# Kernel tuning notes

Hardware: AMD Instinct MI355X
Metric: run time of the kernel (lower is better)

## Reference

```python
import jax, jax.numpy as jnp
import numpy as np
import math

DIM = 1024
MLP = 4096
D_STATE = 16
D_CONV = 4
EXPAND = 2
D_INNER = EXPAND * DIM
HALF = D_INNER // 2
DT_RANK = math.ceil(DIM / 16)
BSZ = 2
SEQ = 2048
LN_EPS = 1e-5


def setup_inputs() -> dict:
    key = jax.random.key(0)
    ks = jax.random.split(key, 12)
    s = lambda k, shape, sc: jax.random.normal(k, shape, dtype=jnp.float32) * sc
    return {
        "x": s(ks[0], (BSZ, SEQ, DIM), 1.0),
        "ln1_g": jnp.ones((DIM,), jnp.float32),
        "ln1_b": jnp.zeros((DIM,), jnp.float32),
        "in_proj_w": s(ks[1], (D_INNER, DIM), 0.02),
        "conv_x_w": s(ks[2], (HALF, 1, D_CONV), 0.1),
        "conv_x_b": jnp.zeros((HALF,), jnp.float32),
        "conv_z_w": s(ks[3], (HALF, 1, D_CONV), 0.1),
        "conv_z_b": jnp.zeros((HALF,), jnp.float32),
        "x_proj_w": s(ks[4], (DT_RANK + 2 * D_STATE, HALF), 0.02),
        "dt_proj_w": s(ks[5], (HALF, DT_RANK), 0.02),
        "dt_proj_b": s(ks[6], (HALF,), 0.1),
        "A_log": jnp.log(jnp.tile(jnp.arange(1, D_STATE + 1, dtype=jnp.float32), (HALF, 1))),
        "Dp": jnp.ones((HALF,), jnp.float32),
        "out_proj_w": s(ks[7], (DIM, D_INNER), 0.02),
        "ln2_g": jnp.ones((DIM,), jnp.float32),
        "ln2_b": jnp.zeros((DIM,), jnp.float32),
        "mlp_w1": s(ks[8], (MLP, DIM), 0.02),
        "mlp_b1": jnp.zeros((MLP,), jnp.float32),
        "mlp_w2": s(ks[9], (DIM, MLP), 0.02),
        "mlp_b2": jnp.zeros((DIM,), jnp.float32),
    }


def _ln(x, g, b):
    mu = jnp.mean(x, -1, keepdims=True)
    v = jnp.mean((x - mu) ** 2, -1, keepdims=True)
    return (x - mu) * jax.lax.rsqrt(v + LN_EPS) * g + b


def _dwconv_same(x, w, b):
    # x: [B, C, L]; w: [C, 1, K] depthwise; PyTorch 'same' pads left=(K-1)//2, right=rest
    total = D_CONV - 1
    left = total // 2
    y = jax.lax.conv_general_dilated(
        x, w, (1,), [(left, total - left)],
        dimension_numbers=("NCH", "OIH", "NCH"),
        feature_group_count=x.shape[1])
    return y + b[None, :, None]


def _mixer(x, in_proj_w, conv_x_w, conv_x_b, conv_z_w, conv_z_b,
           x_proj_w, dt_proj_w, dt_proj_b, A_log, Dp, out_proj_w):
    Bsz = x.shape[0]
    xz = jnp.einsum('bld,ed->ble', x, in_proj_w)              # [B,L,2*HALF]
    xs, zs = jnp.split(xz, 2, axis=-1)
    xc = jax.nn.silu(_dwconv_same(jnp.swapaxes(xs, 1, 2), conv_x_w, conv_x_b))  # [B,HALF,L]
    zc = jax.nn.silu(_dwconv_same(jnp.swapaxes(zs, 1, 2), conv_z_w, conv_z_b))  # [B,HALF,L]
    u = jnp.swapaxes(xc, 1, 2)                                 # [B,L,HALF]
    x_dbl = jnp.einsum('bld,ed->ble', u, x_proj_w)             # [B,L,dt_rank+2N]
    dt, Bm, Cm = jnp.split(x_dbl, [DT_RANK, DT_RANK + D_STATE], axis=-1)
    delta = jax.nn.softplus(jnp.einsum('blr,dr->bld', dt, dt_proj_w) + dt_proj_b)  # [B,L,HALF]
    A = -jnp.exp(A_log)                                        # [HALF,N]
    dA = jnp.exp(jnp.einsum('bld,dn->lbdn', delta, A))         # [L,B,HALF,N]
    dBu = jnp.einsum('bld,bln,bld->lbdn', delta, Bm, u)        # [L,B,HALF,N]
    Cs = jnp.moveaxis(Cm, 1, 0)                                # [L,B,N]

    def step(h, t):
        dA_t, dBu_t, c_t = t
        h = dA_t * h + dBu_t                                   # [B,HALF,N]
        return h, jnp.einsum('bdn,bn->bd', h, c_t)

    h0 = jnp.zeros((Bsz, HALF, D_STATE), x.dtype)
    _, ys = jax.lax.scan(step, h0, (dA, dBu, Cs))              # ys: [L,B,HALF]
    y = jnp.moveaxis(ys, 0, 1) + u * Dp                        # [B,L,HALF]
    y = jnp.concatenate([y, jnp.swapaxes(zc, 1, 2)], axis=-1)  # [B,L,2*HALF]
    return jnp.einsum('ble,de->bld', y, out_proj_w)


def reference(x, ln1_g, ln1_b, in_proj_w, conv_x_w, conv_x_b, conv_z_w, conv_z_b,
              x_proj_w, dt_proj_w, dt_proj_b, A_log, Dp, out_proj_w,
              ln2_g, ln2_b, mlp_w1, mlp_b1, mlp_w2, mlp_b2):
    x = x + _mixer(_ln(x, ln1_g, ln1_b), in_proj_w, conv_x_w, conv_x_b,
                   conv_z_w, conv_z_b, x_proj_w, dt_proj_w, dt_proj_b,
                   A_log, Dp, out_proj_w)
    h = _ln(x, ln2_g, ln2_b)
    h = jax.nn.gelu(jnp.einsum('bld,md->blm', h, mlp_w1) + mlp_b1, approximate=False)
    h = jnp.einsum('blm,dm->bld', h, mlp_w2) + mlp_b2
    return x + h
```

## Files before the change

### kernel.cpp

```cpp
#include <hip/hip_runtime.h>
#include <math.h>

#define DIMD    1024
#define MLPD    4096
#define DSTATE  16
#define DCONV   4
#define HALF    1024
#define DINNER  2048
#define DTRANK  64
#define BSZ     2
#define SEQ     2048
#define NTOK    (BSZ*SEQ)
#define NCH     64
#define CL      (SEQ/NCH)

typedef short bf16x8 __attribute__((ext_vector_type(8)));
typedef float f32x4  __attribute__((ext_vector_type(4)));
typedef float f32x16 __attribute__((ext_vector_type(16)));
typedef unsigned short u16;
typedef unsigned int   u32;
typedef unsigned short u16x4 __attribute__((ext_vector_type(4)));

__device__ __forceinline__ u16 f2bf(float x) {
    union { float f; unsigned int u; } v; v.f = x;
    unsigned int r = (v.u + 0x7FFFu + ((v.u >> 16) & 1u)) >> 16;
    return (u16)r;
}
__device__ __forceinline__ float bf2f(u16 x) {
    union { unsigned int u; float f; } v; v.u = ((unsigned int)x) << 16;
    return v.f;
}

#define SZ_WIN  (DINNER*DIMD)
#define SZ_WXP  (96*HALF)
#define SZ_WDT  (HALF*DTRANK)
#define SZ_WOUT (DIMD*DINNER)
#define SZ_WM1  (MLPD*DIMD)
#define SZ_WM2  (DIMD*MLPD)
#define SZ_TOT  (SZ_WIN+SZ_WXP+SZ_WDT+SZ_WOUT+SZ_WM1+SZ_WM2)
#define CVT_BLOCKS (SZ_TOT / 1024)

__global__ __launch_bounds__(256) void cvtln_kernel(
        const float* __restrict__ x, const float* __restrict__ g,
        const float* __restrict__ b, u16* __restrict__ xn_bf,
        const float* __restrict__ s0, u16* __restrict__ d0,
        const float* __restrict__ s1, u16* __restrict__ d1,
        const float* __restrict__ s2, u16* __restrict__ d2,
        const float* __restrict__ s3, u16* __restrict__ d3,
        const float* __restrict__ s4, u16* __restrict__ d4,
        const float* __restrict__ s5, u16* __restrict__ d5) {
    if (blockIdx.x >= NTOK) {
        int i = (blockIdx.x - NTOK) * 1024 + threadIdx.x * 4;
        #define CVT4(s, d) { \
            float4 v = *(const float4*)((s) + i); \
            u16x4 o; o[0]=f2bf(v.x); o[1]=f2bf(v.y); o[2]=f2bf(v.z); o[3]=f2bf(v.w); \
            *(u16x4*)((d) + i) = o; }
        if (i < SZ_WIN)  { CVT4(s0, d0); return; }  i -= SZ_WIN;
        if (i < SZ_WXP)  { CVT4(s1, d1); return; }  i -= SZ_WXP;
        if (i < SZ_WDT)  { CVT4(s2, d2); return; }  i -= SZ_WDT;
        if (i < SZ_WOUT) { CVT4(s3, d3); return; }  i -= SZ_WOUT;
        if (i < SZ_WM1)  { CVT4(s4, d4); return; }  i -= SZ_WM1;
        if (i < SZ_WM2)  { CVT4(s5, d5); }
        #undef CVT4
        return;
    }
    __shared__ float sm[4];
    int row = blockIdx.x;
    int t = threadIdx.x;
    const float4* xr = (const float4*)(x + (size_t)row * DIMD);
    float4 v = xr[t];
    float s = v.x + v.y + v.z + v.w;
    for (int off = 32; off > 0; off >>= 1) s += __shfl_down(s, off, 64);
    if ((t & 63) == 0) sm[t >> 6] = s;
    __syncthreads();
    float mu = (sm[0] + sm[1] + sm[2] + sm[3]) * (1.0f / DIMD);
    float dx = v.x - mu, dy = v.y - mu, dz = v.z - mu, dw = v.w - mu;
    float ss = dx*dx + dy*dy + dz*dz + dw*dw;
    for (int off = 32; off > 0; off >>= 1) ss += __shfl_down(ss, off, 64);
    __syncthreads();
    if ((t & 63) == 0) sm[t >> 6] = ss;
    __syncthreads();
    float var = (sm[0] + sm[1] + sm[2] + sm[3]) * (1.0f / DIMD);
    float rs = rsqrtf(var + 1e-5f);
    float4 gv = ((const float4*)g)[t];
    float4 bv = ((const float4*)b)[t];
    u16* o = xn_bf + (size_t)row * DIMD + t * 4;
    o[0] = f2bf(dx * rs * gv.x + bv.x);
    o[1] = f2bf(dy * rs * gv.y + bv.y);
    o[2] = f2bf(dz * rs * gv.z + bv.z);
    o[3] = f2bf(dw * rs * gv.w + bv.w);
}

__global__ __launch_bounds__(256) void gemm_small_kernel(
        const u16* __restrict__ A, int lda,
        const u16* __restrict__ W, int K, int N,
        float* __restrict__ Cf, u16* __restrict__ Cb) {
    __shared__ f32x4 red[2][64];
    int t = threadIdx.x;
    int w = t >> 6, lane = t & 63;
    int mt = w & 1, kh = w >> 1;
    int m0 = blockIdx.x * 32 + mt * 16;
    int n0 = blockIdx.y * 16;
    int r = lane & 15, quad = lane >> 4;
    int Kh = K >> 1;
    f32x4 acc = {0.f, 0.f, 0.f, 0.f};
    const u16* ap = A + (size_t)(m0 + r) * lda + kh * Kh + quad * 8;
    const u16* wp = W + (size_t)(n0 + r) * K   + kh * Kh + quad * 8;
    for (int k = 0; k < Kh; k += 32) {
        bf16x8 av = *(const bf16x8*)(ap + k);
        bf16x8 bv = *(const bf16x8*)(wp + k);
        acc = __builtin_amdgcn_mfma_f32_16x16x32_bf16(av, bv, acc, 0, 0, 0);
    }
    if (kh == 1) red[mt][lane] = acc;
    __syncthreads();
    if (kh == 0) {
        f32x4 o = red[mt][lane];
        int col = n0 + r;
        #pragma unroll
        for (int i = 0; i < 4; ++i) {
            int row = m0 + quad * 4 + i;
            size_t idx = (size_t)row * N + col;
            float v = acc[i] + o[i];
            Cf[idx] = v;
            Cb[idx] = f2bf(v);
        }
    }
}

template<int EPI, int TN, int KS>
__global__ __launch_bounds__(256) void gemm128_kernel(
        const u16* __restrict__ A, int lda, const u16* __restrict__ W,
        int K, int N,
        const float* __restrict__ bias, const float* __restrict__ resid,
        float* __restrict__ Cf, float* __restrict__ Cf2,
        u16* __restrict__ Cb) {
    constexpr int NF = TN / 32;
    constexpr int NN = TN / 64;
    __shared__ u16 As0[128 * 32], As1[128 * 32];
    __shared__ u16 Bs0[TN * 32],  Bs1[TN * 32];
    const int t = threadIdx.x;
    const int w = t >> 6;
    const int lane = t & 63;
    const int r32 = lane & 31;
    const int kh  = lane >> 5;
    const int wm = w & 1, wn = w >> 1;
    const int m0 = blockIdx.x * 128;
    const int n0 = blockIdx.y * TN;
    const int Kloc = K / KS;
    const int kz = (KS == 2) ? blockIdx.z : 0;

    f32x16 acc[2][NN];
    #pragma unroll
    for (int mi = 0; mi < 2; ++mi)
        #pragma unroll
        for (int ni = 0; ni < NN; ++ni)
            acc[mi][ni] = (f32x16){0.f,0.f,0.f,0.f,0.f,0.f,0.f,0.f,
                                   0.f,0.f,0.f,0.f,0.f,0.f,0.f,0.f};

    const u16* pa[2];
    const u16* pb[NF / 2];
    #pragma unroll
    for (int i = 0; i < 2; ++i) {
        int c = (i * 4 + w) * 64 + lane;
        int row = c >> 2;
        int q = (c & 3) ^ ((row >> 1) & 3);
        pa[i] = A + (size_t)(m0 + row) * lda + (size_t)kz * Kloc + q * 8;
    }
    #pragma unroll
    for (int i = 0; i < NF / 2; ++i) {
        int c = (i * 4 + w) * 64 + lane;
        int row = c >> 2;
        int q = (c & 3) ^ ((row >> 1) & 3);
        pb[i] = W + (size_t)(n0 + row) * K + (size_t)kz * Kloc + q * 8;
    }
    const int gsw = (r32 >> 1) & 3;
    int aoff[2][2], boff[NN][2];
    #pragma unroll
    for (int mi = 0; mi < 2; ++mi)
        #pragma unroll
        for (int tt = 0; tt < 2; ++tt)
            aoff[mi][tt] = (wm * 64 + mi * 32 + r32) * 32 +
                           ((tt * 2 + kh) ^ gsw) * 8;
    #pragma unroll
    for (int ni = 0; ni < NN; ++ni)
        #pragma unroll
        for (int tt = 0; tt < 2; ++tt)
            boff[ni][tt] = (wn * (TN / 2) + ni * 32 + r32) * 32 +
                           ((tt * 2 + kh) ^ gsw) * 8;

    auto stage = [&](u16* __restrict__ Ad, u16* __restrict__ Bd) {
        #pragma unroll
        for (int i = 0; i < 2; ++i) {
            __builtin_amdgcn_global_load_lds(
                (const __attribute__((address_space(1))) u32*)pa[i],
                (__attribute__((address_space(3))) u32*)(Ad + (i * 4 + w) * 512),
                16, 0, 0);
            pa[i] += 32;
        }
        #pragma unroll
        for (int i = 0; i < NF / 2; ++i) {
            __builtin_amdgcn_global_load_lds(
                (const __attribute__((address_space(1))) u32*)pb[i],
                (__attribute__((address_space(3))) u32*)(Bd + (i * 4 + w) * 512),
                16, 0, 0);
            pb[i] += 32;
        }
    };
    auto compute = [&](const u16* __restrict__ Ab, const u16* __restrict__ Bb) {
        bf16x8 af[2][2], bfr[NN][2];
        #pragma unroll
        for (int mi = 0; mi < 2; ++mi)
            #pragma unroll
            for (int tt = 0; tt < 2; ++tt)
                af[mi][tt] = *(const bf16x8*)(Ab + aoff[mi][tt]);
        #pragma unroll
        for (int ni = 0; ni < NN; ++ni)
            #pragma unroll
            for (int tt = 0; tt < 2; ++tt)
                bfr[ni][tt] = *(const bf16x8*)(Bb + boff[ni][tt]);
        #pragma unroll
        for (int tt = 0; tt < 2; ++tt)
            #pragma unroll
            for (int mi = 0; mi < 2; ++mi)
                #pragma unroll
                for (int ni = 0; ni < NN; ++ni)
                    acc[mi][ni] = __builtin_amdgcn_mfma_f32_32x32x16_bf16(
                        af[mi][tt], bfr[ni][tt], acc[mi][ni], 0, 0, 0);
    };

    stage(As0, Bs0);
    for (int k0 = 0; k0 < Kloc; k0 += 64) {
        __syncthreads();
        if (k0 + 32 < Kloc) stage(As1, Bs1);
        compute(As0, Bs0);
        __syncthreads();
        if (k0 + 64 < Kloc) stage(As0, Bs0);
        compute(As1, Bs1);
    }

    float* Cfo = (KS == 2 && kz) ? Cf2 : Cf;
    #pragma unroll
    for (int mi = 0; mi < 2; ++mi) {
        #pragma unroll
        for (int ni = 0; ni < NN; ++ni) {
            #pragma unroll
            for (int reg = 0; reg < 16; ++reg) {
                int row = m0 + wm * 64 + mi * 32 + (reg & 3) + 8 * (reg >> 2) + 4 * kh;
                int col = n0 + wn * (TN / 2) + ni * 32 + r32;
                size_t idx = (size_t)row * N + col;
                float v = acc[mi][ni][reg];
                if (EPI == 1) { v += bias[col]; v = (v > 20.f) ? v : log1pf(expf(v)); }
                if (EPI == 2) {
                    v += bias[col];
                    float e = __expf(fminf(1.5957691216f * v + 0.0713548162f * v * v * v, 80.f));
                    v = v * __fdividef(e, e + 1.f);
                }
                if (EPI == 3) { v += resid[idx]; }
                if (EPI == 4) { v += bias[col] + resid[idx]; }
                if (EPI == 2 || EPI == 5) Cb[idx] = f2bf(v);
                else                      Cfo[idx] = v;
            }
        }
    }
}

__global__ __launch_bounds__(256) void reduce2_kernel(
        const float* __restrict__ P0, const float* __restrict__ P1,
        const float* __restrict__ bias, const float* __restrict__ resid,
        float* __restrict__ out) {
    size_t idx = ((size_t)blockIdx.x * 256 + threadIdx.x) * 4;
    float4 a = *(const float4*)(P0 + idx);
    float4 b = *(const float4*)(P1 + idx);
    float4 rr = *(const float4*)(resid + idx);
    int col = (int)(idx & (DIMD - 1));
    float4 bb = *(const float4*)(bias + col);
    float4 o;
    o.x = a.x + b.x + rr.x + bb.x;
    o.y = a.y + b.y + rr.y + bb.y;
    o.z = a.z + b.z + rr.z + bb.z;
    o.w = a.w + b.w + rr.w + bb.w;
    *(float4*)(out + idx) = o;
}

__global__ __launch_bounds__(256) void reduce_ln_kernel(
        const float* __restrict__ P0, const float* __restrict__ P1,
        const float* __restrict__ resid,
        const float* __restrict__ g, const float* __restrict__ b,
        float* __restrict__ x2, u16* __restrict__ out_bf) {
    __shared__ float sm[4];
    int row = blockIdx.x;
    int t = threadIdx.x;
    size_t base = (size_t)row * DIMD + t * 4;
    float4 a  = *(const float4*)(P0 + base);
    float4 p  = *(const float4*)(P1 + base);
    float4 rr = *(const float4*)(resid + base);
    float4 v;
    v.x = a.x + p.x + rr.x;
    v.y = a.y + p.y + rr.y;
    v.z = a.z + p.z + rr.z;
    v.w = a.w + p.w + rr.w;
    *(float4*)(x2 + base) = v;
    float s = v.x + v.y + v.z + v.w;
    for (int off = 32; off > 0; off >>= 1) s += __shfl_down(s, off, 64);
    if ((t & 63) == 0) sm[t >> 6] = s;
    __syncthreads();
    float mu = (sm[0] + sm[1] + sm[2] + sm[3]) * (1.0f / DIMD);
    float dx = v.x - mu, dy = v.y - mu, dz = v.z - mu, dw = v.w - mu;
    float ss = dx*dx + dy*dy + dz*dz + dw*dw;
    for (int off = 32; off > 0; off >>= 1) ss += __shfl_down(ss, off, 64);
    __syncthreads();
    if ((t & 63) == 0) sm[t >> 6] = ss;
    __syncthreads();
    float var = (sm[0] + sm[1] + sm[2] + sm[3]) * (1.0f / DIMD);
    float rs = rsqrtf(var + 1e-5f);
    float4 gv = ((const float4*)g)[t];
    float4 bv = ((const float4*)b)[t];
    u16* o = out_bf + base;
    o[0] = f2bf(dx * rs * gv.x + bv.x);
    o[1] = f2bf(dy * rs * gv.y + bv.y);
    o[2] = f2bf(dz * rs * gv.z + bv.z);
    o[3] = f2bf(dw * rs * gv.w + bv.w);
}

__global__ __launch_bounds__(256) void conv_silu_kernel(
        const u16* __restrict__ xz,
        const float* __restrict__ wx, const float* __restrict__ bx,
        const float* __restrict__ wz, const float* __restrict__ bz,
        u16* __restrict__ u_bf, u16* __restrict__ ycat) {
    int c  = blockIdx.x * 256 + threadIdx.x;
    int gy = blockIdx.y;
    int b  = gy >> 8;
    int l0 = (gy & 255) * 8;
    const u16* base = xz + ((size_t)(b * SEQ + l0)) * DINNER;
    float wxr[4], wzr[4];
    #pragma unroll
    for (int k = 0; k < 4; ++k) { wxr[k] = wx[c * 4 + k]; wzr[k] = wz[c * 4 + k]; }
    float bxv = bx[c], bzv = bz[c];
    float xm1 = (l0 > 0) ? bf2f(base[c - DINNER]) : 0.f;
    float x0v = bf2f(base[c]);
    float x1v = bf2f(base[c + DINNER]);
    float zm1 = (l0 > 0) ? bf2f(base[HALF + c - DINNER]) : 0.f;
    float z0v = bf2f(base[HALF + c]);
    float z1v = bf2f(base[HALF + c + DINNER]);
    u16* up = u_bf + ((size_t)(b * SEQ + l0)) * HALF + c;
    u16* yp = ycat + ((size_t)(b * SEQ + l0)) * DINNER + HALF + c;
    #pragma unroll
    for (int l = 0; l < 8; ++l) {
        bool in = (l0 + l + 2) < SEQ;
        float x2v = in ? bf2f(base[(size_t)(l + 2) * DINNER + c]) : 0.f;
        float z2v = in ? bf2f(base[(size_t)(l + 2) * DINNER + HALF + c]) : 0.f;
        float ax = bxv + wxr[0]*xm1 + wxr[1]*x0v + wxr[2]*x1v + wxr[3]*x2v;
        float az = bzv + wzr[0]*zm1 + wzr[1]*z0v + wzr[2]*z1v + wzr[3]*z2v;
        float sx = ax * __fdividef(1.f, 1.f + __expf(-ax));
        float sz = az * __fdividef(1.f, 1.f + __expf(-az));
        *up = f2bf(sx); *yp = f2bf(sz);
        up += HALF; yp += DINNER;
        xm1 = x0v; x0v = x1v; x1v = x2v;
        zm1 = z0v; z0v = z1v; z1v = z2v;
    }
}

__global__ __launch_bounds__(256) void scan_p1_kernel(
        const float* __restrict__ delta, const u16* __restrict__ u_bf,
        const float* __restrict__ x_dbl, const float* __restrict__ A_log,
        float* __restrict__ hfin, float* __restrict__ dsum) {
    int t  = blockIdx.x * 256 + threadIdx.x;
    int d  = t & (HALF - 1);
    int ch = (t >> 10) & (NCH - 1);
    int b  = t >> 16;
    float Ac[16], h[16];
    #pragma unroll
    for (int i = 0; i < 4; ++i) {
        float4 a = *(const float4*)&A_log[d * DSTATE + i * 4];
        Ac[4*i+0] = -__expf(a.x); Ac[4*i+1] = -__expf(a.y);
        Ac[4*i+2] = -__expf(a.z); Ac[4*i+3] = -__expf(a.w);
        h[4*i+0] = 0.f; h[4*i+1] = 0.f; h[4*i+2] = 0.f; h[4*i+3] = 0.f;
    }
    int l0 = b * SEQ + ch * CL;
    size_t off = (size_t)l0 * HALF + d;
    const float* xrow = x_dbl + (size_t)l0 * 96;
    float ds = 0.f;
    #pragma unroll 4
    for (int l = 0; l < CL; ++l) {
        float dl = delta[off];
        float uv = bf2f(u_bf[off]);
        off += HALF;
        float4 B0 = *(const float4*)(xrow + 64);
        float4 B1 = *(const float4*)(xrow + 68);
        float4 B2 = *(const float4*)(xrow + 72);
        float4 B3 = *(const float4*)(xrow + 76);
        xrow += 96;
        float dBu = dl * uv;
        ds += dl;
        float Bv[16] = {B0.x,B0.y,B0.z,B0.w, B1.x,B1.y,B1.z,B1.w,
                        B2.x,B2.y,B2.z,B2.w, B3.x,B3.y,B3.z,B3.w};
        #pragma unroll
        for (int n = 0; n < 16; ++n)
            h[n] = __expf(dl * Ac[n]) * h[n] + dBu * Bv[n];
    }
    float4* hf = (float4*)&hfin[(size_t)t * 16];
    #pragma unroll
    for (int i = 0; i < 4; ++i)
        hf[i] = (float4){h[4*i+0], h[4*i+1], h[4*i+2], h[4*i+3]};
    dsum[t] = ds;
}

__global__ __launch_bounds__(256) void scan_p2_kernel(
        const float* __restrict__ A_log, const float* __restrict__ dsum,
        const float* __restrict__ hfin, float* __restrict__ hin) {
    int t = blockIdx.x * 256 + threadIdx.x;
    int n = t & 15;
    int d = (t >> 4) & (HALF - 1);
    int b = t >> 14;
    float Ac = -__expf(A_log[d * DSTATE + n]);
    float h = 0.f;
    for (int ch = 0; ch < NCH; ++ch) {
        size_t chain = ((size_t)(b * NCH + ch) * HALF) + d;
        hin[chain * 16 + n] = h;
        float ds = dsum[chain];
        h = __expf(Ac * ds) * h + hfin[chain * 16 + n];
    }
}

__global__ __launch_bounds__(256) void scan_p3_kernel(
        const float* __restrict__ delta, const u16* __restrict__ u_bf,
        const float* __restrict__ x_dbl, const float* __restrict__ A_log,
        const float* __restrict__ Dp, const float* __restrict__ hin,
        u16* __restrict__ ycat) {
    int t  = blockIdx.x * 256 + threadIdx.x;
    int d  = t & (HALF - 1);
    int ch = (t >> 10) & (NCH - 1);
    int b  = t >> 16;
    float Ac[16], h[16];
    #pragma unroll
    for (int i = 0; i < 4; ++i) {
        float4 a  = *(const float4*)&A_log[d * DSTATE + i * 4];
        float4 hv = *(const float4*)&hin[(size_t)t * 16 + i * 4];
        Ac[4*i+0] = -__expf(a.x); Ac[4*i+1] = -__expf(a.y);
        Ac[4*i+2] = -__expf(a.z); Ac[4*i+3] = -__expf(a.w);
        h[4*i+0] = hv.x; h[4*i+1] = hv.y; h[4*i+2] = hv.z; h[4*i+3] = hv.w;
    }
    float Dv = Dp[d];
    int l0 = b * SEQ + ch * CL;
    size_t off = (size_t)l0 * HALF + d;
    const float* xrow = x_dbl + (size_t)l0 * 96;
    u16* yp = ycat + (size_t)l0 * DINNER + d;
    #pragma unroll 4
    for (int l = 0; l < CL; ++l) {
        float dl = delta[off];
        float uv = bf2f(u_bf[off]);
        off += HALF;
        float4 B0 = *(const float4*)(xrow + 64);
        float4 B1 = *(const float4*)(xrow + 68);
        float4 B2 = *(const float4*)(xrow + 72);
        float4 B3 = *(const float4*)(xrow + 76);
        float4 C0 = *(const float4*)(xrow + 80);
        float4 C1 = *(const float4*)(xrow + 84);
        float4 C2 = *(const float4*)(xrow + 88);
        float4 C3 = *(const float4*)(xrow + 92);
        xrow += 96;
        float dBu = dl * uv;
        float Bv[16] = {B0.x,B0.y,B0.z,B0.w, B1.x,B1.y,B1.z,B1.w,
                        B2.x,B2.y,B2.z,B2.w, B3.x,B3.y,B3.z,B3.w};
        float Cv[16] = {C0.x,C0.y,C0.z,C0.w, C1.x,C1.y,C1.z,C1.w,
                        C2.x,C2.y,C2.z,C2.w, C3.x,C3.y,C3.z,C3.w};
        float y = uv * Dv;
        #pragma unroll
        for (int n = 0; n < 16; ++n) {
            h[n] = __expf(dl * Ac[n]) * h[n] + dBu * Bv[n];
            y += h[n] * Cv[n];
        }
        *yp = f2bf(y);
        yp += DINNER;
    }
}

extern "C" void kernel_launch(void* const* d_in, const int* in_sizes, int n_in,
                              void* d_out, int out_size, void* d_ws, size_t ws_size,
                              hipStream_t stream) {
    const float* x         = (const float*)d_in[0];
    const float* ln1_g     = (const float*)d_in[1];
    const float* ln1_b     = (const float*)d_in[2];
    const float* in_proj_w = (const float*)d_in[3];
    const float* conv_x_w  = (const float*)d_in[4];
    const float* conv_x_b  = (const float*)d_in[5];
    const float* conv_z_w  = (const float*)d_in[6];
    const float* conv_z_b  = (const float*)d_in[7];
    const float* x_proj_w  = (const float*)d_in[8];
    const float* dt_proj_w = (const float*)d_in[9];
    const float* dt_proj_b = (const float*)d_in[10];
    const float* A_log     = (const float*)d_in[11];
    const float* Dp        = (const float*)d_in[12];
    const float* out_proj_w= (const float*)d_in[13];
    const float* ln2_g     = (const float*)d_in[14];
    const float* ln2_b     = (const float*)d_in[15];
    const float* mlp_w1    = (const float*)d_in[16];
    const float* mlp_b1    = (const float*)d_in[17];
    const float* mlp_w2    = (const float*)d_in[18];
    const float* mlp_b2    = (const float*)d_in[19];
    float* out = (float*)d_out;

    char* p = (char*)d_ws;
    auto alloc = [&](size_t bytes) {
        char* r = p; p += (bytes + 255) & ~(size_t)255; return r;
    };
    u16*   w_in   = (u16*)  alloc((size_t)DINNER * DIMD * 2);
    u16*   w_xp   = (u16*)  alloc((size_t)96 * HALF * 2);
    u16*   w_dt   = (u16*)  alloc((size_t)HALF * DTRANK * 2);
    u16*   w_out  = (u16*)  alloc((size_t)DIMD * DINNER * 2);
    u16*   w_m1   = (u16*)  alloc((size_t)MLPD * DIMD * 2);
    u16*   w_m2   = (u16*)  alloc((size_t)DIMD * MLPD * 2);
    u16*   xn_bf  = (u16*)  alloc((size_t)NTOK * DIMD * 2);
    u16*   xz_bf  = (u16*)  alloc((size_t)NTOK * DINNER * 2);
    u16*   u_bf   = (u16*)  alloc((size_t)NTOK * HALF * 2);
    u16*   ycat   = (u16*)  alloc((size_t)NTOK * DINNER * 2);
    float* x_dbl  = (float*)alloc((size_t)NTOK * 96 * 4);
    u16*   xdbl_bf= (u16*)  alloc((size_t)NTOK * 96 * 2);
    float* delta  = (float*)alloc((size_t)NTOK * HALF * 4);
    float* x2     = (float*)alloc((size_t)NTOK * DIMD * 4);
    u16*   ln2_bf = (u16*)  alloc((size_t)NTOK * DIMD * 2);
    u16*   mlp_h  = (u16*)  alloc((size_t)NTOK * MLPD * 2);
    float* hfin = (float*)mlp_h;
    float* hin  = hfin + (size_t)BSZ * NCH * HALF * DSTATE;
    float* dsum = hin  + (size_t)BSZ * NCH * HALF * DSTATE;
    float* P0 = delta;
    float* P1 = (float*)xz_bf;

    cvtln_kernel<<<NTOK + CVT_BLOCKS, 256, 0, stream>>>(
        x, ln1_g, ln1_b, xn_bf,
        in_proj_w, w_in, x_proj_w, w_xp, dt_proj_w, w_dt,
        out_proj_w, w_out, mlp_w1, w_m1, mlp_w2, w_m2);

    gemm128_kernel<5,128,1><<<dim3(NTOK/128, DINNER/128), 256, 0, stream>>>(
        xn_bf, DIMD, w_in, DIMD, DINNER, nullptr, nullptr, nullptr, nullptr, xz_bf);

    conv_silu_kernel<<<dim3(HALF/256, NTOK/8), 256, 0, stream>>>(
        xz_bf, conv_x_w, conv_x_b, conv_z_w, conv_z_b, u_bf, ycat);

    gemm_small_kernel<<<dim3(NTOK/32, 96/16), 256, 0, stream>>>(
        u_bf, HALF, w_xp, HALF, 96, x_dbl, xdbl_bf);

    gemm128_kernel<1,64,1><<<dim3(NTOK/128, HALF/64), 256, 0, stream>>>(
        xdbl_bf, 96, w_dt, DTRANK, HALF, dt_proj_b, nullptr, delta, nullptr, nullptr);

    scan_p1_kernel<<<(BSZ*NCH*HALF)/256, 256, 0, stream>>>(
        delta, u_bf, x_dbl, A_log, hfin, dsum);
    scan_p2_kernel<<<(BSZ*HALF*DSTATE)/256, 256, 0, stream>>>(
        A_log, dsum, hfin, hin);
    scan_p3_kernel<<<(BSZ*NCH*HALF)/256, 256, 0, stream>>>(
        delta, u_bf, x_dbl, A_log, Dp, hin, ycat);

    gemm128_kernel<0,128,2><<<dim3(NTOK/128, DIMD/128, 2), 256, 0, stream>>>(
        ycat, DINNER, w_out, DINNER, DIMD, nullptr, nullptr, P0, P1, nullptr);
    reduce_ln_kernel<<<NTOK, 256, 0, stream>>>(
        P0, P1, x, ln2_g, ln2_b, x2, ln2_bf);

    gemm128_kernel<2,128,1><<<dim3(NTOK/128, MLPD/128), 256, 0, stream>>>(
        ln2_bf, DIMD, w_m1, DIMD, MLPD, mlp_b1, nullptr, nullptr, nullptr, mlp_h);

    gemm128_kernel<0,128,2><<<dim3(NTOK/128, DIMD/128, 2), 256, 0, stream>>>(
        mlp_h, MLPD, w_m2, MLPD, DIMD, nullptr, nullptr, P0, P1, nullptr);
    reduce2_kernel<<<(NTOK*DIMD)/1024, 256, 0, stream>>>(
        P0, P1, mlp_b2, x2, out);
}
```

Before: 413.0 us.

## Triple-buffer GEMM shared-memory tiles with partial vmcnt waits

Moves the bf16 GEMM main loop from double to triple buffering of the A/B LDS tiles, staging two tiles ahead. Plain __syncthreads are replaced by explicit s_waitcnt vmcnt(N) followed by a raw barrier, so that global loads for the next stage can stay in flight while the current tile is computed. The cost is more LDS per block, which may reduce occupancy. Correctness also depends on the hand-counted vmcnt values matching the number of loads issued per stage.

```diff
diff --git a/kernel.cpp b/kernel.cpp
--- a/kernel.cpp
+++ b/kernel.cpp
@@ -136,8 +136,8 @@
         u16* __restrict__ Cb) {
     constexpr int NF = TN / 32;
     constexpr int NN = TN / 64;
-    __shared__ u16 As0[128 * 32], As1[128 * 32];
-    __shared__ u16 Bs0[TN * 32],  Bs1[TN * 32];
+    __shared__ u16 As0[128 * 32], As1[128 * 32], As2[128 * 32];
+    __shared__ u16 Bs0[TN * 32],  Bs1[TN * 32],  Bs2[TN * 32];
     const int t = threadIdx.x;
     const int w = t >> 6;
     const int lane = t & 63;
@@ -227,15 +227,35 @@
                     acc[mi][ni] = __builtin_amdgcn_mfma_f32_32x32x16_bf16(
                         af[mi][tt], bfr[ni][tt], acc[mi][ni], 0, 0, 0);
     };
+    auto waitbar = [&](bool last) {
+        if (last) {
+            asm volatile("s_waitcnt vmcnt(0)" ::: "memory");
+        } else if constexpr (TN == 128) {
+            asm volatile("s_waitcnt vmcnt(4)" ::: "memory");
+        } else {
+            asm volatile("s_waitcnt vmcnt(3)" ::: "memory");
+        }
+        __builtin_amdgcn_s_barrier();
+        __builtin_amdgcn_sched_barrier(0);
+    };
 
     stage(As0, Bs0);
-    for (int k0 = 0; k0 < Kloc; k0 += 64) {
-        __syncthreads();
-        if (k0 + 32 < Kloc) stage(As1, Bs1);
+    stage(As1, Bs1);
+    const int NT = Kloc / 32;
+    int it = 0;
+    while (true) {
+        waitbar(it == NT - 1);
+        if (it + 2 < NT) stage(As2, Bs2);
         compute(As0, Bs0);
-        __syncthreads();
-        if (k0 + 64 < Kloc) stage(As0, Bs0);
+        if (++it >= NT) break;
+        waitbar(it == NT - 1);
+        if (it + 2 < NT) stage(As0, Bs0);
         compute(As1, Bs1);
+        if (++it >= NT) break;
+        waitbar(it == NT - 1);
+        if (it + 2 < NT) stage(As1, Bs1);
+        compute(As2, Bs2);
+        if (++it >= NT) break;
     }
 
     float* Cfo = (KS == 2 && kz) ? Cf2 : Cf;
```

Measured after the change: 421.1 us. About the same (+2.0%).
